# Kernel tuning notes

Measured on AMD Instinct MI355X. Metric: run time of the kernel, lower is better.

## Reference

```python
import jax, jax.numpy as jnp
import numpy as np

EMBED = 64
HEADS = 8
HEAD_DIM = EMBED // HEADS
B, N, T = 8, 128, 64


def setup_inputs() -> dict:
    key = jax.random.key(0)
    ks = jax.random.split(key, 8)
    shp = (B, N, T, EMBED)
    values = jax.random.normal(ks[0], shp, dtype=jnp.float32)
    keys = jax.random.normal(ks[1], shp, dtype=jnp.float32)
    query = jax.random.normal(ks[2], shp, dtype=jnp.float32)
    s = 1.0 / np.sqrt(HEAD_DIM)
    Wv = jax.random.normal(ks[3], (HEAD_DIM, HEAD_DIM), dtype=jnp.float32) * s
    Wk = jax.random.normal(ks[4], (HEAD_DIM, HEAD_DIM), dtype=jnp.float32) * s
    Wq = jax.random.normal(ks[5], (HEAD_DIM, HEAD_DIM), dtype=jnp.float32) * s
    so = 1.0 / np.sqrt(EMBED)
    Wo = jax.random.normal(ks[6], (EMBED, EMBED), dtype=jnp.float32) * so
    bo = jax.random.normal(ks[7], (EMBED,), dtype=jnp.float32) * 0.01
    return {"values": values, "keys": keys, "query": query,
            "Wv": Wv, "Wk": Wk, "Wq": Wq, "Wo": Wo, "bo": bo}


def reference(values, keys, query, Wv, Wk, Wq, Wo, bo):
    b, n, t, c = query.shape
    h, d = HEADS, HEAD_DIM
    # split heads: (B,N,T,H,D)
    v = values.reshape(b, n, t, h, d)
    k = keys.reshape(b, n, t, h, d)
    q = query.reshape(b, n, t, h, d)
    # per-head linear projections (torch Linear: x @ W.T, no bias)
    v = jnp.einsum('bnthd,ed->bnthe', v, Wv)
    k = jnp.einsum('bnthd,ed->bnthe', k, Wk)
    q = jnp.einsum('bnthd,ed->bnthe', q, Wq)
    # attention over spatial axis N, independent per (t, h)
    energy = jnp.einsum('bqthd,bkthd->bqkth', q, k)  # (B,N,N,T,H)
    attn = jax.nn.softmax(energy / jnp.sqrt(jnp.float32(c)), axis=2)
    out = jnp.einsum('bqkth,bkthd->bqthd', attn, v).reshape(b, n, t, h * d)
    # fc_out: x @ Wo.T + bo
    return out @ Wo.T + bo
```

## Files before the change

kernel.cpp:

```cpp
#include <hip/hip_runtime.h>


typedef _Float16 half4 __attribute__((ext_vector_type(4)));
typedef float    f32x4 __attribute__((ext_vector_type(4)));

#define MFMA16(a,b,c) __builtin_amdgcn_mfma_f32_16x16x16f16((a),(b),(c),0,0,0)

__device__ __forceinline__ unsigned short f2h(float f){
    union { _Float16 h; unsigned short u; } c; c.h = (_Float16)f; return c.u;
}
__device__ __forceinline__ float dot4(const float4 a, const float4 b){
    return a.x*b.x + a.y*b.y + a.z*b.z + a.w*b.w;
}

#define ZS 0
#define OS 8
#define MB 16
#define KB 144
#define QB 8336
#define VB 16528
#define CB 25296
#define WB 34000
#define LDS_TOTAL 38352

__global__ __launch_bounds__(512, 4)
void sattn_kernel(const float* __restrict__ V,
                  const float* __restrict__ K,
                  const float* __restrict__ Q,
                  const float* __restrict__ Wv,
                  const float* __restrict__ Wk,
                  const float* __restrict__ Wq,
                  const float* __restrict__ Wo,
                  const float* __restrict__ bo,
                  float* __restrict__ Out)
{
    __shared__ __align__(16) unsigned short smem[LDS_TOTAL];

    const int tid  = threadIdx.x;
    const int bid  = blockIdx.x;
    const int b    = bid >> 6;
    const int t    = bid & 63;
    const long base = (long)b * 524288 + t * 64;
    const float SC = 0.18033688011112043f;

    const int cn0 = tid >> 3, ch = tid & 7;

    const float* p0 = K + base + cn0*4096 + ch*8;
    const float* p1 = V + base + cn0*4096 + ch*8;
    const float* p2 = Q + base + cn0*4096 + ch*8;
    float4 k0a = *(const float4*)p0,          k0b = *(const float4*)(p0+4);
    float4 v0a = *(const float4*)p1,          v0b = *(const float4*)(p1+4);
    float4 q0a = *(const float4*)p2,          q0b = *(const float4*)(p2+4);
    float4 k1a = *(const float4*)(p0+262144), k1b = *(const float4*)(p0+262148);
    float4 v1a = *(const float4*)(p1+262144), v1b = *(const float4*)(p1+262148);
    float4 q1a = *(const float4*)(p2+262144), q1b = *(const float4*)(p2+262148);

    if (tid < 4)      *(unsigned int*)(smem + tid*2) = 0u;
    else if (tid < 8) *(unsigned int*)(smem + tid*2) = 0x3C003C00u;

    {
        const int o = tid >> 3, g = tid & 7;
        const float* ws = Wo + o*64 + g*8;
        float4 woa = *(const float4*)ws;
        float4 wob = *(const float4*)(ws + 4);
        float wo8[8] = {woa.x, woa.y, woa.z, woa.w, wob.x, wob.y, wob.z, wob.w};
        float w2[8] = {0,0,0,0,0,0,0,0};
        #pragma unroll
        for (int e = 0; e < 8; ++e){
            float4 wv0 = *(const float4*)(Wv + e*8);
            float4 wv1 = *(const float4*)(Wv + e*8 + 4);
            float we = wo8[e];
            w2[0] += we*wv0.x; w2[1] += we*wv0.y; w2[2] += we*wv0.z; w2[3] += we*wv0.w;
            w2[4] += we*wv1.x; w2[5] += we*wv1.y; w2[6] += we*wv1.z; w2[7] += we*wv1.w;
        }
        half4 h0; h0.x=(_Float16)w2[0]; h0.y=(_Float16)w2[1]; h0.z=(_Float16)w2[2]; h0.w=(_Float16)w2[3];
        half4 h1; h1.x=(_Float16)w2[4]; h1.y=(_Float16)w2[5]; h1.z=(_Float16)w2[6]; h1.w=(_Float16)w2[7];
        *(half4*)(smem + WB + o*68 + g*8)     = h0;
        *(half4*)(smem + WB + o*68 + g*8 + 4) = h1;
    }

    if (tid < 64){
        const int dd = tid & 7;
        const int dp = tid >> 3;
        float m = 0.f;
        #pragma unroll
        for (int e = 0; e < 8; ++e)
            m += Wk[e*8 + dd] * Wq[e*8 + dp];
        reinterpret_cast<float*>(smem + MB)[tid] = m * SC;
    }

    {
        half4 h0; h0.x=(_Float16)q0a.x; h0.y=(_Float16)q0a.y; h0.z=(_Float16)q0a.z; h0.w=(_Float16)q0a.w;
        half4 h1; h1.x=(_Float16)q0b.x; h1.y=(_Float16)q0b.y; h1.z=(_Float16)q0b.z; h1.w=(_Float16)q0b.w;
        *(half4*)(smem + QB + ch*1024 + cn0*8)     = h0;
        *(half4*)(smem + QB + ch*1024 + cn0*8 + 4) = h1;
        half4 h2; h2.x=(_Float16)q1a.x; h2.y=(_Float16)q1a.y; h2.z=(_Float16)q1a.z; h2.w=(_Float16)q1a.w;
        half4 h3; h3.x=(_Float16)q1b.x; h3.y=(_Float16)q1b.y; h3.z=(_Float16)q1b.z; h3.w=(_Float16)q1b.w;
        *(half4*)(smem + QB + ch*1024 + (cn0+64)*8)     = h2;
        *(half4*)(smem + QB + ch*1024 + (cn0+64)*8 + 4) = h3;
    }

    {
        unsigned short* vb = smem + VB + ch*1096;
        vb[0*136 + cn0] = f2h(v0a.x); vb[1*136 + cn0] = f2h(v0a.y);
        vb[2*136 + cn0] = f2h(v0a.z); vb[3*136 + cn0] = f2h(v0a.w);
        vb[4*136 + cn0] = f2h(v0b.x); vb[5*136 + cn0] = f2h(v0b.y);
        vb[6*136 + cn0] = f2h(v0b.z); vb[7*136 + cn0] = f2h(v0b.w);
        vb[0*136 + cn0+64] = f2h(v1a.x); vb[1*136 + cn0+64] = f2h(v1a.y);
        vb[2*136 + cn0+64] = f2h(v1a.z); vb[3*136 + cn0+64] = f2h(v1a.w);
        vb[4*136 + cn0+64] = f2h(v1b.x); vb[5*136 + cn0+64] = f2h(v1b.y);
        vb[6*136 + cn0+64] = f2h(v1b.z); vb[7*136 + cn0+64] = f2h(v1b.w);
    }

    __syncthreads();

    {
        const float* mt = reinterpret_cast<const float*>(smem + MB);
        float4 m0[8], m1[8];
        #pragma unroll
        for (int dp = 0; dp < 8; ++dp){
            m0[dp] = *(const float4*)(mt + dp*8);
            m1[dp] = *(const float4*)(mt + dp*8 + 4);
        }
        float ok[8];
        #pragma unroll
        for (int dp = 0; dp < 8; ++dp)
            ok[dp] = dot4(k0a, m0[dp]) + dot4(k0b, m1[dp]);
        half4 h0; h0.x=(_Float16)ok[0]; h0.y=(_Float16)ok[1]; h0.z=(_Float16)ok[2]; h0.w=(_Float16)ok[3];
        half4 h1; h1.x=(_Float16)ok[4]; h1.y=(_Float16)ok[5]; h1.z=(_Float16)ok[6]; h1.w=(_Float16)ok[7];
        *(half4*)(smem + KB + ch*1024 + cn0*8)     = h0;
        *(half4*)(smem + KB + ch*1024 + cn0*8 + 4) = h1;
        #pragma unroll
        for (int dp = 0; dp < 8; ++dp)
            ok[dp] = dot4(k1a, m0[dp]) + dot4(k1b, m1[dp]);
        half4 h2; h2.x=(_Float16)ok[0]; h2.y=(_Float16)ok[1]; h2.z=(_Float16)ok[2]; h2.w=(_Float16)ok[3];
        half4 h3; h3.x=(_Float16)ok[4]; h3.y=(_Float16)ok[5]; h3.z=(_Float16)ok[6]; h3.w=(_Float16)ok[7];
        *(half4*)(smem + KB + ch*1024 + (cn0+64)*8)     = h2;
        *(half4*)(smem + KB + ch*1024 + (cn0+64)*8 + 4) = h3;
    }

    __syncthreads();

    const int h    = tid >> 6;
    const int q16  = tid & 15;
    const int quad = (tid & 63) >> 4;
    const f32x4 zz = {0.f, 0.f, 0.f, 0.f};

    half4 kf[8];
    #pragma unroll
    for (int mt = 0; mt < 8; ++mt){
        int a = KB + h*1024 + (mt*16 + q16)*8 + quad*4;
        if (quad >= 2) a = ZS;
        kf[mt] = *(const half4*)(smem + a);
    }
    half4 vf[8];
    #pragma unroll
    for (int s = 0; s < 8; ++s){
        int a = VB + h*1096 + q16*136 + s*16 + quad*4;
        if (q16 > 8)  a = ZS;
        if (q16 == 8) a = OS;
        vf[s] = *(const half4*)(smem + a);
    }

    #pragma unroll 1
    for (int qs = 0; qs < 8; ++qs){
        int qa = QB + h*1024 + (qs*16 + q16)*8 + quad*4;
        if (quad >= 2) qa = ZS;
        half4 qf = *(const half4*)(smem + qa);

        half4 pf[8];

        {
            f32x4 acc[4];
            #pragma unroll
            for (int mt = 0; mt < 4; ++mt)
                acc[mt] = MFMA16(kf[mt], qf, zz);
            #pragma unroll
            for (int mt = 0; mt < 4; ++mt){
                pf[mt].x = (_Float16)__builtin_amdgcn_exp2f(acc[mt][0]);
                pf[mt].y = (_Float16)__builtin_amdgcn_exp2f(acc[mt][1]);
                pf[mt].z = (_Float16)__builtin_amdgcn_exp2f(acc[mt][2]);
                pf[mt].w = (_Float16)__builtin_amdgcn_exp2f(acc[mt][3]);
            }
        }
        {
            f32x4 acc[4];
            #pragma unroll
            for (int mt = 0; mt < 4; ++mt)
                acc[mt] = MFMA16(kf[mt+4], qf, zz);
            #pragma unroll
            for (int mt = 0; mt < 4; ++mt){
                pf[mt+4].x = (_Float16)__builtin_amdgcn_exp2f(acc[mt][0]);
                pf[mt+4].y = (_Float16)__builtin_amdgcn_exp2f(acc[mt][1]);
                pf[mt+4].z = (_Float16)__builtin_amdgcn_exp2f(acc[mt][2]);
                pf[mt+4].w = (_Float16)__builtin_amdgcn_exp2f(acc[mt][3]);
            }
        }

        f32x4 o0 = zz, o1 = zz;
        #pragma unroll
        for (int s8 = 0; s8 < 4; ++s8){
            o0 = MFMA16(pf[s8],     vf[s8],     o0);
            o1 = MFMA16(pf[s8 + 4], vf[s8 + 4], o1);
        }

        float tr[4];
        #pragma unroll
        for (int r = 0; r < 4; ++r)
            tr[r] = o0[r] + o1[r];

        const int dl = (tid & 48) + 8;
        float invr[4];
        #pragma unroll
        for (int r = 0; r < 4; ++r)
            invr[r] = __builtin_amdgcn_rcpf(__shfl(tr[r], dl, 64));

        if (q16 < 8){
            #pragma unroll
            for (int r = 0; r < 4; ++r){
                int row = qs*16 + quad*4 + r;
                smem[CB + row*68 + h*8 + q16] = f2h(tr[r] * invr[r]);
            }
        }
    }

    __syncthreads();

    const int w = h;
    half4 af[4];
    #pragma unroll
    for (int ks = 0; ks < 4; ++ks)
        af[ks] = *(const half4*)(smem + CB + (w*16 + q16)*68 + ks*16 + quad*4);

    #pragma unroll
    for (int nt = 0; nt < 4; ++nt){
        f32x4 a = zz;
        #pragma unroll
        for (int ks = 0; ks < 4; ++ks){
            half4 bf = *(const half4*)(smem + WB + (nt*16 + q16)*68 + ks*16 + quad*4);
            a = MFMA16(af[ks], bf, a);
        }
        float bb = bo[nt*16 + q16];
        #pragma unroll
        for (int r = 0; r < 4; ++r){
            int row = w*16 + quad*4 + r;
            Out[base + (long)row*4096 + nt*16 + q16] = a[r] + bb;
        }
    }
}

extern "C" void kernel_launch(void* const* d_in, const int* in_sizes, int n_in,
                              void* d_out, int out_size, void* d_ws, size_t ws_size,
                              hipStream_t stream)
{
    const float* V  = (const float*)d_in[0];
    const float* K  = (const float*)d_in[1];
    const float* Q  = (const float*)d_in[2];
    const float* Wv = (const float*)d_in[3];
    const float* Wk = (const float*)d_in[4];
    const float* Wq = (const float*)d_in[5];
    const float* Wo = (const float*)d_in[6];
    const float* bo = (const float*)d_in[7];

    sattn_kernel<<<dim3(512), dim3(512), 0, stream>>>(
        V, K, Q, Wv, Wk, Wq, Wo, bo, (float*)d_out);
}
```

Before: 109.5 us.

## Double block size to 1024 threads and split query tiles across wave pairs

Each block now runs 1024 threads. Each thread loads one row of K/V/Q instead of two, and each head gets two waves that each take half of the query tiles. The fc_out stage splits its output column tiles across wave pairs. K and V fragments are now reloaded from LDS inside the query loop instead of being held in registers, which cuts register pressure. The aim is more memory-level parallelism and more resident waves, paid for with extra LDS reads per iteration.

```diff
diff --git a/kernel.cpp b/kernel.cpp
--- a/kernel.cpp
+++ b/kernel.cpp
@@ -23,7 +23,7 @@
 #define WB 34000
 #define LDS_TOTAL 38352
 
-__global__ __launch_bounds__(512, 4)
+__global__ __launch_bounds__(1024, 8)
 void sattn_kernel(const float* __restrict__ V,
                   const float* __restrict__ K,
                   const float* __restrict__ Q,
@@ -43,22 +43,20 @@
     const long base = (long)b * 524288 + t * 64;
     const float SC = 0.18033688011112043f;
 
-    const int cn0 = tid >> 3, ch = tid & 7;
-
-    const float* p0 = K + base + cn0*4096 + ch*8;
-    const float* p1 = V + base + cn0*4096 + ch*8;
-    const float* p2 = Q + base + cn0*4096 + ch*8;
-    float4 k0a = *(const float4*)p0,          k0b = *(const float4*)(p0+4);
-    float4 v0a = *(const float4*)p1,          v0b = *(const float4*)(p1+4);
-    float4 q0a = *(const float4*)p2,          q0b = *(const float4*)(p2+4);
-    float4 k1a = *(const float4*)(p0+262144), k1b = *(const float4*)(p0+262148);
-    float4 v1a = *(const float4*)(p1+262144), v1b = *(const float4*)(p1+262148);
-    float4 q1a = *(const float4*)(p2+262144), q1b = *(const float4*)(p2+262148);
+    const int cn = tid >> 3;
+    const int ch = tid & 7;
+
+    const float* p0 = K + base + cn*4096 + ch*8;
+    const float* p1 = V + base + cn*4096 + ch*8;
+    const float* p2 = Q + base + cn*4096 + ch*8;
+    float4 ka = *(const float4*)p0, kb = *(const float4*)(p0+4);
+    float4 va = *(const float4*)p1, vb_ = *(const float4*)(p1+4);
+    float4 qa = *(const float4*)p2, qb_ = *(const float4*)(p2+4);
 
     if (tid < 4)      *(unsigned int*)(smem + tid*2) = 0u;
     else if (tid < 8) *(unsigned int*)(smem + tid*2) = 0x3C003C00u;
 
-    {
+    if (tid < 512){
         const int o = tid >> 3, g = tid & 7;
         const float* ws = Wo + o*64 + g*8;
         float4 woa = *(const float4*)ws;
@@ -90,91 +88,69 @@
     }
 
     {
-        half4 h0; h0.x=(_Float16)q0a.x; h0.y=(_Float16)q0a.y; h0.z=(_Float16)q0a.z; h0.w=(_Float16)q0a.w;
-        half4 h1; h1.x=(_Float16)q0b.x; h1.y=(_Float16)q0b.y; h1.z=(_Float16)q0b.z; h1.w=(_Float16)q0b.w;
-        *(half4*)(smem + QB + ch*1024 + cn0*8)     = h0;
-        *(half4*)(smem + QB + ch*1024 + cn0*8 + 4) = h1;
-        half4 h2; h2.x=(_Float16)q1a.x; h2.y=(_Float16)q1a.y; h2.z=(_Float16)q1a.z; h2.w=(_Float16)q1a.w;
-        half4 h3; h3.x=(_Float16)q1b.x; h3.y=(_Float16)q1b.y; h3.z=(_Float16)q1b.z; h3.w=(_Float16)q1b.w;
-        *(half4*)(smem + QB + ch*1024 + (cn0+64)*8)     = h2;
-        *(half4*)(smem + QB + ch*1024 + (cn0+64)*8 + 4) = h3;
+        half4 h0; h0.x=(_Float16)qa.x; h0.y=(_Float16)qa.y; h0.z=(_Float16)qa.z; h0.w=(_Float16)qa.w;
+        half4 h1; h1.x=(_Float16)qb_.x; h1.y=(_Float16)qb_.y; h1.z=(_Float16)qb_.z; h1.w=(_Float16)qb_.w;
+        *(half4*)(smem + QB + ch*1024 + cn*8)     = h0;
+        *(half4*)(smem + QB + ch*1024 + cn*8 + 4) = h1;
     }
 
     {
         unsigned short* vb = smem + VB + ch*1096;
-        vb[0*136 + cn0] = f2h(v0a.x); vb[1*136 + cn0] = f2h(v0a.y);
-        vb[2*136 + cn0] = f2h(v0a.z); vb[3*136 + cn0] = f2h(v0a.w);
-        vb[4*136 + cn0] = f2h(v0b.x); vb[5*136 + cn0] = f2h(v0b.y);
-        vb[6*136 + cn0] = f2h(v0b.z); vb[7*136 + cn0] = f2h(v0b.w);
-        vb[0*136 + cn0+64] = f2h(v1a.x); vb[1*136 + cn0+64] = f2h(v1a.y);
-        vb[2*136 + cn0+64] = f2h(v1a.z); vb[3*136 + cn0+64] = f2h(v1a.w);
-        vb[4*136 + cn0+64] = f2h(v1b.x); vb[5*136 + cn0+64] = f2h(v1b.y);
-        vb[6*136 + cn0+64] = f2h(v1b.z); vb[7*136 + cn0+64] = f2h(v1b.w);
+        vb[0*136 + cn] = f2h(va.x); vb[1*136 + cn] = f2h(va.y);
+        vb[2*136 + cn] = f2h(va.z); vb[3*136 + cn] = f2h(va.w);
+        vb[4*136 + cn] = f2h(vb_.x); vb[5*136 + cn] = f2h(vb_.y);
+        vb[6*136 + cn] = f2h(vb_.z); vb[7*136 + cn] = f2h(vb_.w);
     }
 
     __syncthreads();
 
     {
         const float* mt = reinterpret_cast<const float*>(smem + MB);
-        float4 m0[8], m1[8];
+        float ok[8];
         #pragma unroll
         for (int dp = 0; dp < 8; ++dp){
-            m0[dp] = *(const float4*)(mt + dp*8);
-            m1[dp] = *(const float4*)(mt + dp*8 + 4);
-        }
-        float ok[8];
-        #pragma unroll
-        for (int dp = 0; dp < 8; ++dp)
-            ok[dp] = dot4(k0a, m0[dp]) + dot4(k0b, m1[dp]);
+            float4 m0 = *(const float4*)(mt + dp*8);
+            float4 m1 = *(const float4*)(mt + dp*8 + 4);
+            ok[dp] = dot4(ka, m0) + dot4(kb, m1);
+        }
         half4 h0; h0.x=(_Float16)ok[0]; h0.y=(_Float16)ok[1]; h0.z=(_Float16)ok[2]; h0.w=(_Float16)ok[3];
         half4 h1; h1.x=(_Float16)ok[4]; h1.y=(_Float16)ok[5]; h1.z=(_Float16)ok[6]; h1.w=(_Float16)ok[7];
-        *(half4*)(smem + KB + ch*1024 + cn0*8)     = h0;
-        *(half4*)(smem + KB + ch*1024 + cn0*8 + 4) = h1;
-        #pragma unroll
-        for (int dp = 0; dp < 8; ++dp)
-            ok[dp] = dot4(k1a, m0[dp]) + dot4(k1b, m1[dp]);
-        half4 h2; h2.x=(_Float16)ok[0]; h2.y=(_Float16)ok[1]; h2.z=(_Float16)ok[2]; h2.w=(_Float16)ok[3];
-        half4 h3; h3.x=(_Float16)ok[4]; h3.y=(_Float16)ok[5]; h3.z=(_Float16)ok[6]; h3.w=(_Float16)ok[7];
-        *(half4*)(smem + KB + ch*1024 + (cn0+64)*8)     = h2;
-        *(half4*)(smem + KB + ch*1024 + (cn0+64)*8 + 4) = h3;
+        *(half4*)(smem + KB + ch*1024 + cn*8)     = h0;
+        *(half4*)(smem + KB + ch*1024 + cn*8 + 4) = h1;
     }
 
     __syncthreads();
 
-    const int h    = tid >> 6;
-    const int q16  = tid & 15;
-    const int quad = (tid & 63) >> 4;
+    const int wid  = tid >> 6;
+    const int h    = wid >> 1;
+    const int qh   = wid & 1;
+    const int lane = tid & 63;
+    const int q16  = lane & 15;
+    const int quad = lane >> 4;
     const f32x4 zz = {0.f, 0.f, 0.f, 0.f};
 
-    half4 kf[8];
-    #pragma unroll
-    for (int mt = 0; mt < 8; ++mt){
-        int a = KB + h*1024 + (mt*16 + q16)*8 + quad*4;
-        if (quad >= 2) a = ZS;
-        kf[mt] = *(const half4*)(smem + a);
-    }
-    half4 vf[8];
-    #pragma unroll
-    for (int s = 0; s < 8; ++s){
-        int a = VB + h*1096 + q16*136 + s*16 + quad*4;
-        if (q16 > 8)  a = ZS;
-        if (q16 == 8) a = OS;
-        vf[s] = *(const half4*)(smem + a);
-    }
-
     #pragma unroll 1
-    for (int qs = 0; qs < 8; ++qs){
-        int qa = QB + h*1024 + (qs*16 + q16)*8 + quad*4;
-        if (quad >= 2) qa = ZS;
-        half4 qf = *(const half4*)(smem + qa);
+    for (int qs4 = 0; qs4 < 4; ++qs4){
+        const int qs = qh*4 + qs4;
+
+        int qadr = QB + h*1024 + (qs*16 + q16)*8 + quad*4;
+        if (quad >= 2) qadr = ZS;
+        half4 qf = *(const half4*)(smem + qadr);
 
         half4 pf[8];
 
         {
+            half4 kfa[4];
+            #pragma unroll
+            for (int mt = 0; mt < 4; ++mt){
+                int a = KB + h*1024 + (mt*16 + q16)*8 + quad*4;
+                if (quad >= 2) a = ZS;
+                kfa[mt] = *(const half4*)(smem + a);
+            }
             f32x4 acc[4];
             #pragma unroll
             for (int mt = 0; mt < 4; ++mt)
-                acc[mt] = MFMA16(kf[mt], qf, zz);
+                acc[mt] = MFMA16(kfa[mt], qf, zz);
             #pragma unroll
             for (int mt = 0; mt < 4; ++mt){
                 pf[mt].x = (_Float16)__builtin_amdgcn_exp2f(acc[mt][0]);
@@ -184,10 +160,17 @@
             }
         }
         {
+            half4 kfa[4];
+            #pragma unroll
+            for (int mt = 0; mt < 4; ++mt){
+                int a = KB + h*1024 + ((mt+4)*16 + q16)*8 + quad*4;
+                if (quad >= 2) a = ZS;
+                kfa[mt] = *(const half4*)(smem + a);
+            }
             f32x4 acc[4];
             #pragma unroll
             for (int mt = 0; mt < 4; ++mt)
-                acc[mt] = MFMA16(kf[mt+4], qf, zz);
+                acc[mt] = MFMA16(kfa[mt], qf, zz);
             #pragma unroll
             for (int mt = 0; mt < 4; ++mt){
                 pf[mt+4].x = (_Float16)__builtin_amdgcn_exp2f(acc[mt][0]);
@@ -198,10 +181,31 @@
         }
 
         f32x4 o0 = zz, o1 = zz;
-        #pragma unroll
-        for (int s8 = 0; s8 < 4; ++s8){
-            o0 = MFMA16(pf[s8],     vf[s8],     o0);
-            o1 = MFMA16(pf[s8 + 4], vf[s8 + 4], o1);
+        {
+            half4 vfa[4];
+            #pragma unroll
+            for (int s = 0; s < 4; ++s){
+                int a = VB + h*1096 + q16*136 + s*16 + quad*4;
+                if (q16 > 8)  a = ZS;
+                if (q16 == 8) a = OS;
+                vfa[s] = *(const half4*)(smem + a);
+            }
+            #pragma unroll
+            for (int s = 0; s < 4; ++s)
+                o0 = MFMA16(pf[s], vfa[s], o0);
+        }
+        {
+            half4 vfa[4];
+            #pragma unroll
+            for (int s = 0; s < 4; ++s){
+                int a = VB + h*1096 + q16*136 + (s+4)*16 + quad*4;
+                if (q16 > 8)  a = ZS;
+                if (q16 == 8) a = OS;
+                vfa[s] = *(const half4*)(smem + a);
+            }
+            #pragma unroll
+            for (int s = 0; s < 4; ++s)
+                o1 = MFMA16(pf[s+4], vfa[s], o1);
         }
 
         float tr[4];
@@ -209,7 +213,7 @@
         for (int r = 0; r < 4; ++r)
             tr[r] = o0[r] + o1[r];
 
-        const int dl = (tid & 48) + 8;
+        const int dl = (lane & 48) + 8;
         float invr[4];
         #pragma unroll
         for (int r = 0; r < 4; ++r)
@@ -226,14 +230,17 @@
 
     __syncthreads();
 
-    const int w = h;
+    const int rt  = wid >> 1;
+    const int ntb = (wid & 1) * 2;
+
     half4 af[4];
     #pragma unroll
     for (int ks = 0; ks < 4; ++ks)
-        af[ks] = *(const half4*)(smem + CB + (w*16 + q16)*68 + ks*16 + quad*4);
+        af[ks] = *(const half4*)(smem + CB + (rt*16 + q16)*68 + ks*16 + quad*4);
 
     #pragma unroll
-    for (int nt = 0; nt < 4; ++nt){
+    for (int j = 0; j < 2; ++j){
+        const int nt = ntb + j;
         f32x4 a = zz;
         #pragma unroll
         for (int ks = 0; ks < 4; ++ks){
@@ -243,7 +250,7 @@
         float bb = bo[nt*16 + q16];
         #pragma unroll
         for (int r = 0; r < 4; ++r){
-            int row = w*16 + quad*4 + r;
+            int row = rt*16 + quad*4 + r;
             Out[base + (long)row*4096 + nt*16 + q16] = a[r] + bb;
         }
     }
@@ -262,6 +269,6 @@
     const float* Wo = (const float*)d_in[6];
     const float* bo = (const float*)d_in[7];
 
-    sattn_kernel<<<dim3(512), dim3(512), 0, stream>>>(
+    sattn_kernel<<<dim3(512), dim3(1024), 0, stream>>>(
         V, K, Q, Wv, Wk, Wq, Wo, bo, (float*)d_out);
 }
```

After: 111.8 us. +2.1%, slower.
